# Performance work log

Measured on AMD Instinct MI355X. Metric: run time of the kernel, lower is better.

## Reference

```python
import jax, jax.numpy as jnp
import numpy as np

NUM_CLUSTERS = 8
KMEANS_ITERS = 10  # fixed Lloyd iterations (deterministic stand-in for sklearn KMeans)


def _pairwise_sqdist(x, cent):
    # x: [N, C], cent: [K, C] -> [N, K]
    return (jnp.sum(x * x, axis=1, keepdims=True)
            - 2.0 * (x @ cent.T)
            + jnp.sum(cent * cent, axis=1)[None, :])


def _kmeans_labels(x):
    # x: [N, C] -> labels [N] int32. Deterministic init: first K points.
    K = NUM_CLUSTERS
    cent0 = x[:K]

    def step(cent, _):
        d = _pairwise_sqdist(x, cent)                      # [N, K]
        lab = jnp.argmin(d, axis=1)                        # [N]
        oh = jax.nn.one_hot(lab, K, dtype=x.dtype)         # [N, K]
        cnt = oh.sum(axis=0)                               # [K]
        sums = oh.T @ x                                    # [K, C]
        new = jnp.where(cnt[:, None] > 0,
                        sums / jnp.maximum(cnt, 1.0)[:, None],
                        cent)
        return new, None

    cent, _ = jax.lax.scan(step, cent0, None, length=KMEANS_ITERS)
    return jnp.argmin(_pairwise_sqdist(x, cent), axis=1)


def setup_inputs() -> dict:
    key = jax.random.key(0)
    feature_map = jax.random.normal(key, (32, 256, 64, 64), dtype=jnp.float32)
    return {"feature_map": feature_map}


def reference(feature_map):
    B, C, H, W = feature_map.shape
    K = NUM_CLUSTERS
    # (B, C, H, W) -> (B, N, C) with N = H*W
    feats = feature_map.reshape(B, C, H * W).transpose(0, 2, 1)
    # Cluster assignments are non-differentiable constants (torch uses .detach())
    labels = jax.vmap(_kmeans_labels)(jax.lax.stop_gradient(feats))   # [B, N]
    oh = jax.nn.one_hot(labels, K, dtype=feats.dtype)                 # [B, N, K]
    cnt = oh.sum(axis=1)                                              # [B, K]
    sums = jnp.einsum('bnk,bnc->bkc', oh, feats)                      # [B, K, C]
    # empty cluster -> zeros, matching torch fallback
    clustered = jnp.where(cnt[..., None] > 0,
                          sums / jnp.maximum(cnt, 1.0)[..., None],
                          0.0)
    return clustered  # [B, K, C]
```

## Files before the change

kernel.cpp:

```cpp
#include <hip/hip_runtime.h>
#include <stdint.h>

#define NB   32
#define NC   256
#define NPTS 4096
#define KCL  8
#define KC   384
#define NPANEL 11
#define BSTRIDE 388

__device__ float np_sumsq_avx512(const float* sh) {
  float half[2];
  #pragma unroll
  for (int h = 0; h < 2; ++h) {
    const float* ap = sh + h * 128;
    float rv[16];
    #pragma unroll
    for (int l = 0; l < 16; ++l) {
      float q[8];
      #pragma unroll
      for (int j = 0; j < 8; ++j) {
        float e = ap[16 * j + l];
        q[j] = __fmul_rn(e, e);
      }
      rv[l] = __fadd_rn(__fadd_rn(__fadd_rn(q[0], q[1]), __fadd_rn(q[2], q[3])),
                        __fadd_rn(__fadd_rn(q[4], q[5]), __fadd_rn(q[6], q[7])));
    }
    float t1[8];
    #pragma unroll
    for (int l = 0; l < 8; ++l) t1[l] = __fadd_rn(rv[l], rv[l + 8]);
    float t2[4];
    #pragma unroll
    for (int l = 0; l < 4; ++l) t2[l] = __fadd_rn(t1[l], t1[l + 2 + 2]);
    float t3[2];
    #pragma unroll
    for (int l = 0; l < 2; ++l) t3[l] = __fadd_rn(t2[l], t2[l + 2]);
    half[h] = __fadd_rn(t3[0], t3[1]);
  }
  return __fadd_rn(half[0], half[1]);
}

__global__ __launch_bounds__(256) void k_init(const float* __restrict__ X,
                                              float* __restrict__ centT,
                                              float* __restrict__ cnorm) {
  const int b = blockIdx.x >> 3, k = blockIdx.x & 7, c = threadIdx.x;
  __shared__ float sarr[NC];
  float v = X[(size_t)b * NC * NPTS + (size_t)c * NPTS + k];
  centT[(b * NC + c) * KCL + k] = v;
  sarr[c] = v;
  __syncthreads();
  if (c == 0) cnorm[b * KCL + k] = np_sumsq_avx512(sarr);
}

__global__ __launch_bounds__(256) void k_assign(const float* __restrict__ X,
                                                const float* __restrict__ centT,
                                                const float* __restrict__ cnorm,
                                                int* __restrict__ lab) {
  const int blk = blockIdx.x;
  const int b   = blk >> 4;
  const int n0  = (blk & 15) << 8;
  const int t   = threadIdx.x;

  const float* Xp = X + (size_t)b * NC * NPTS + n0 + t;
  const float4* cw = (const float4*)(centT + (size_t)b * NC * KCL);

  float cnf[KCL];
  #pragma unroll
  for (int k = 0; k < KCL; ++k) cnf[k] = cnorm[b * KCL + k];

  float a = 0.f;
  float bb[KCL];
  #pragma unroll
  for (int k = 0; k < KCL; ++k) bb[k] = 0.f;

  #pragma unroll 8
  for (int c = 0; c < NC; ++c) {
    float x = Xp[(size_t)c * NPTS];
    a = __fadd_rn(a, __fmul_rn(x, x));
    float4 c0 = cw[c * 2], c1 = cw[c * 2 + 1];
    bb[0] = __builtin_fmaf(x, c0.x, bb[0]);
    bb[1] = __builtin_fmaf(x, c0.y, bb[1]);
    bb[2] = __builtin_fmaf(x, c0.z, bb[2]);
    bb[3] = __builtin_fmaf(x, c0.w, bb[3]);
    bb[4] = __builtin_fmaf(x, c1.x, bb[4]);
    bb[5] = __builtin_fmaf(x, c1.y, bb[5]);
    bb[6] = __builtin_fmaf(x, c1.z, bb[6]);
    bb[7] = __builtin_fmaf(x, c1.w, bb[7]);
  }

  int lb = 0; float best = 3.4e38f;
  #pragma unroll
  for (int k = 0; k < KCL; ++k) {
    float d = __fadd_rn(__fsub_rn(a, __fmul_rn(2.0f, bb[k])), cnf[k]);
    if (d < best) { best = d; lb = k; }
  }
  lab[b * NPTS + n0 + t] = lb;
}

__global__ __launch_bounds__(256) void k_psum(const float* __restrict__ X,
                                              const int* __restrict__ lab,
                                              float* __restrict__ pp,
                                              int* __restrict__ pc) {
  const int blk = blockIdx.x;
  const int b = blk / 88, r = blk % 88, panel = r >> 3, cg = r & 7;
  const int p0 = panel * KC;
  const int len = (panel < 10) ? KC : (NPTS - 10 * KC);
  const int t = threadIdx.x, k = t & 7, cl = t >> 3, lane = t & 63;

  __shared__ __align__(16) float buf[32 * BSTRIDE];
  __shared__ int perm[KC];
  __shared__ int wcnt[6][KCL];
  __shared__ int cbase[6][KCL];
  __shared__ int offs[KCL], hist[KCL];

  const float* Xb = X + (size_t)b * NC * NPTS + (size_t)(cg * 32) * NPTS + p0;
  if (len == KC) {
    #pragma unroll
    for (int i2 = 0; i2 < 12; ++i2) {
      int i = i2 * 256 + t;
      int c = i / 96, q4 = i - c * 96;
      float4 v = *(const float4*)(Xb + (size_t)c * NPTS + q4 * 4);
      *(float4*)&buf[c * BSTRIDE + q4 * 4] = v;
    }
  } else {
    #pragma unroll
    for (int i2 = 0; i2 < 8; ++i2) {
      int i = i2 * 256 + t;
      int c = i >> 6, q4 = i & 63;
      float4 v = *(const float4*)(Xb + (size_t)c * NPTS + q4 * 4);
      *(float4*)&buf[c * BSTRIDE + q4 * 4] = v;
    }
  }

  const int* Lb = lab + b * NPTS + p0;
  const uint64_t lt = (1ull << lane) - 1ull;
  int ml0, ml1, rk0 = 0, rk1 = 0;
  {
    const int q = t;
    ml0 = (q < len) ? Lb[q] : -1;
    const int chunk = q >> 6;
    #pragma unroll
    for (int kk = 0; kk < KCL; ++kk) {
      uint64_t m = __ballot(ml0 == kk);
      if (lane == 0) wcnt[chunk][kk] = (int)__popcll(m);
      if (ml0 == kk) rk0 = (int)__popcll(m & lt);
    }
  }
  {
    const int q = 256 + t;
    ml1 = (q < len) ? Lb[q] : -1;
    const int chunk = q >> 6;
    #pragma unroll
    for (int kk = 0; kk < KCL; ++kk) {
      uint64_t m = __ballot(ml1 == kk);
      if (lane == 0 && chunk < 6) wcnt[chunk][kk] = (int)__popcll(m);
      if (ml1 == kk) rk1 = (int)__popcll(m & lt);
    }
  }
  __syncthreads();
  if (t == 0) {
    int rr = 0;
    for (int kk = 0; kk < KCL; ++kk) {
      int s = 0;
      #pragma unroll
      for (int ch = 0; ch < 6; ++ch) { cbase[ch][kk] = rr + s; s += wcnt[ch][kk]; }
      offs[kk] = rr; hist[kk] = s; rr += s;
    }
  }
  __syncthreads();
  if (ml0 >= 0) perm[cbase[t >> 6][ml0] + rk0] = t;
  if (ml1 >= 0) perm[cbase[(256 + t) >> 6][ml1] + rk1] = 256 + t;
  __syncthreads();

  const int base = offs[k], n = hist[k];
  const float* bp = &buf[cl * BSTRIDE];
  float pa = 0.f;
  #pragma unroll 4
  for (int i = 0; i < n; ++i) {
    int p = perm[base + i];
    pa = __fadd_rn(pa, bp[p]);
  }
  pp[(size_t)((b * NPANEL + panel) * KCL + k) * NC + cg * 32 + cl] = pa;
  if (cl == 0) pc[(b * NPANEL + panel) * KCL + k] = n;
}

__global__ __launch_bounds__(256) void k_combine(const float* __restrict__ pp,
                                                 const int* __restrict__ pc,
                                                 float* __restrict__ centT,
                                                 float* __restrict__ cnorm) {
  const int b = blockIdx.x >> 3, k = blockIdx.x & 7, c = threadIdx.x;
  float C = 0.f;
  int cnt = 0;
  for (int pnl = 0; pnl < NPANEL; ++pnl) {
    C = __fadd_rn(C, pp[(size_t)((b * NPANEL + pnl) * KCL + k) * NC + c]);
    cnt += pc[(b * NPANEL + pnl) * KCL + k];
  }
  const float mean = __fdiv_rn(C, (float)((cnt > 0) ? cnt : 1));
  const int ci = (b * NC + c) * KCL + k;
  float nv = (cnt > 0) ? mean : centT[ci];
  centT[ci] = nv;
  __shared__ float sarr[NC];
  sarr[c] = nv;
  __syncthreads();
  if (c == 0) cnorm[b * KCL + k] = np_sumsq_avx512(sarr);
}

__global__ __launch_bounds__(256) void k_out(const float* __restrict__ pp,
                                             const int* __restrict__ pc,
                                             float* __restrict__ out) {
  const int b = blockIdx.x >> 3, k = blockIdx.x & 7, c = threadIdx.x;
  float C = 0.f;
  int cnt = 0;
  for (int pnl = 0; pnl < NPANEL; ++pnl) {
    C = __fadd_rn(C, pp[(size_t)((b * NPANEL + pnl) * KCL + k) * NC + c]);
    cnt += pc[(b * NPANEL + pnl) * KCL + k];
  }
  out[(b * KCL + k) * NC + c] =
      (cnt > 0) ? __fdiv_rn(C, (float)cnt) : 0.0f;
}

extern "C" void kernel_launch(void* const* d_in, const int* in_sizes, int n_in,
                              void* d_out, int out_size, void* d_ws, size_t ws_size,
                              hipStream_t stream) {
  const float* X = (const float*)d_in[0];
  float* out = (float*)d_out;

  float* centT = (float*)d_ws;
  float* cnorm = centT + (size_t)NB * NC * KCL;
  int*   lab   = (int*)(cnorm + NB * KCL);
  float* pp    = (float*)(lab + (size_t)NB * NPTS);
  int*   pc    = (int*)(pp + (size_t)NB * NPANEL * KCL * NC);

  k_init<<<NB * KCL, 256, 0, stream>>>(X, centT, cnorm);
  for (int it = 0; it < 10; ++it) {
    k_assign<<<NB * 16, 256, 0, stream>>>(X, centT, cnorm, lab);
    k_psum<<<NB * NPANEL * KCL, 256, 0, stream>>>(X, lab, pp, pc);
    k_combine<<<NB * KCL, 256, 0, stream>>>(pp, pc, centT, cnorm);
  }
  k_assign<<<NB * 16, 256, 0, stream>>>(X, centT, cnorm, lab);
  k_psum<<<NB * NPANEL * KCL, 256, 0, stream>>>(X, lab, pp, pc);
  k_out<<<NB * KCL, 256, 0, stream>>>(pp, pc, out);
}
```

Baseline: 741.1 us.

## Fuse centroid update into assign kernel and halve psum shared buffer

Removes the separate k_combine kernel. Each assign block now recomputes the new centroids and their norms from the panel partial sums, stages the centroids in shared memory, and ping-pongs between two centroid buffers. k_psum now loads its panel in two halves into a half-sized shared buffer, which lowers LDS use and should allow more blocks per CU, at the cost of extra barriers. The work of combining centroids is repeated by the 16 blocks per batch, and the norm is computed by only 8 threads per block.

```diff
diff --git a/kernel.cpp b/kernel.cpp
--- a/kernel.cpp
+++ b/kernel.cpp
@@ -7,7 +7,8 @@
 #define KCL  8
 #define KC   384
 #define NPANEL 11
-#define BSTRIDE 388
+#define HALF0 192
+#define BSTR  196
 
 __device__ float np_sumsq_avx512(const float* sh) {
   float half[2];
@@ -40,44 +41,106 @@
   return __fadd_rn(half[0], half[1]);
 }
 
+__device__ float np_sumsq_avx512_s8(const float* base, int k) {
+  float half[2];
+  #pragma unroll
+  for (int h = 0; h < 2; ++h) {
+    float rv[16];
+    #pragma unroll
+    for (int l = 0; l < 16; ++l) {
+      float q[8];
+      #pragma unroll
+      for (int j = 0; j < 8; ++j) {
+        float e = base[(h * 128 + 16 * j + l) * KCL + k];
+        q[j] = __fmul_rn(e, e);
+      }
+      rv[l] = __fadd_rn(__fadd_rn(__fadd_rn(q[0], q[1]), __fadd_rn(q[2], q[3])),
+                        __fadd_rn(__fadd_rn(q[4], q[5]), __fadd_rn(q[6], q[7])));
+    }
+    float t1[8];
+    #pragma unroll
+    for (int l = 0; l < 8; ++l) t1[l] = __fadd_rn(rv[l], rv[l + 8]);
+    float t2[4];
+    #pragma unroll
+    for (int l = 0; l < 4; ++l) t2[l] = __fadd_rn(t1[l], t1[l + 2 + 2]);
+    float t3[2];
+    #pragma unroll
+    for (int l = 0; l < 2; ++l) t3[l] = __fadd_rn(t2[l], t2[l + 2]);
+    half[h] = __fadd_rn(t3[0], t3[1]);
+  }
+  return __fadd_rn(half[0], half[1]);
+}
+
 __global__ __launch_bounds__(256) void k_init(const float* __restrict__ X,
-                                              float* __restrict__ centT,
-                                              float* __restrict__ cnorm) {
+                                              float* __restrict__ cent0,
+                                              float* __restrict__ cnorm0) {
   const int b = blockIdx.x >> 3, k = blockIdx.x & 7, c = threadIdx.x;
   __shared__ float sarr[NC];
   float v = X[(size_t)b * NC * NPTS + (size_t)c * NPTS + k];
-  centT[(b * NC + c) * KCL + k] = v;
+  cent0[(b * NC + c) * KCL + k] = v;
   sarr[c] = v;
   __syncthreads();
-  if (c == 0) cnorm[b * KCL + k] = np_sumsq_avx512(sarr);
+  if (c == 0) cnorm0[b * KCL + k] = np_sumsq_avx512(sarr);
 }
 
 __global__ __launch_bounds__(256) void k_assign(const float* __restrict__ X,
-                                                const float* __restrict__ centT,
-                                                const float* __restrict__ cnorm,
-                                                int* __restrict__ lab) {
+                                                const float* __restrict__ pp,
+                                                const int* __restrict__ pc,
+                                                const float* __restrict__ centPrev,
+                                                float* __restrict__ centCur,
+                                                const float* __restrict__ cnorm0,
+                                                int* __restrict__ lab,
+                                                int it) {
   const int blk = blockIdx.x;
   const int b   = blk >> 4;
   const int n0  = (blk & 15) << 8;
   const int t   = threadIdx.x;
 
+  __shared__ __align__(16) float centL[NC * KCL];
+  __shared__ float cnfL[KCL];
+
+  if (it == 0) {
+    const float4* cp = (const float4*)(centPrev + (size_t)b * NC * KCL);
+    #pragma unroll
+    for (int i2 = 0; i2 < 2; ++i2)
+      ((float4*)centL)[i2 * 256 + t] = cp[i2 * 256 + t];
+    if (t < KCL) cnfL[t] = cnorm0[b * KCL + t];
+  } else {
+    const int c = t;
+    #pragma unroll
+    for (int k = 0; k < KCL; ++k) {
+      float C = 0.f; int cnt = 0;
+      for (int pnl = 0; pnl < NPANEL; ++pnl) {
+        C = __fadd_rn(C, pp[(size_t)((b * NPANEL + pnl) * KCL + k) * NC + c]);
+        cnt += pc[(b * NPANEL + pnl) * KCL + k];
+      }
+      const float mean = __fdiv_rn(C, (float)((cnt > 0) ? cnt : 1));
+      const int ci = (b * NC + c) * KCL + k;
+      float nv = (cnt > 0) ? mean : centPrev[ci];
+      centCur[ci] = nv;
+      centL[c * KCL + k] = nv;
+    }
+    __syncthreads();
+    if (t < KCL) cnfL[t] = np_sumsq_avx512_s8(centL, t);
+  }
+  __syncthreads();
+
+  float cnf[KCL];
+  #pragma unroll
+  for (int k = 0; k < KCL; ++k) cnf[k] = cnfL[k];
+
   const float* Xp = X + (size_t)b * NC * NPTS + n0 + t;
-  const float4* cw = (const float4*)(centT + (size_t)b * NC * KCL);
-
-  float cnf[KCL];
-  #pragma unroll
-  for (int k = 0; k < KCL; ++k) cnf[k] = cnorm[b * KCL + k];
-
   float a = 0.f;
   float bb[KCL];
   #pragma unroll
   for (int k = 0; k < KCL; ++k) bb[k] = 0.f;
+  const float4* cL4 = (const float4*)centL;
 
   #pragma unroll 8
   for (int c = 0; c < NC; ++c) {
     float x = Xp[(size_t)c * NPTS];
     a = __fadd_rn(a, __fmul_rn(x, x));
-    float4 c0 = cw[c * 2], c1 = cw[c * 2 + 1];
+    float4 c0 = cL4[c * 2], c1 = cL4[c * 2 + 1];
     bb[0] = __builtin_fmaf(x, c0.x, bb[0]);
     bb[1] = __builtin_fmaf(x, c0.y, bb[1]);
     bb[2] = __builtin_fmaf(x, c0.z, bb[2]);
@@ -107,29 +170,20 @@
   const int len = (panel < 10) ? KC : (NPTS - 10 * KC);
   const int t = threadIdx.x, k = t & 7, cl = t >> 3, lane = t & 63;
 
-  __shared__ __align__(16) float buf[32 * BSTRIDE];
+  __shared__ __align__(16) float buf[32 * BSTR];
   __shared__ int perm[KC];
   __shared__ int wcnt[6][KCL];
   __shared__ int cbase[6][KCL];
   __shared__ int offs[KCL], hist[KCL];
 
   const float* Xb = X + (size_t)b * NC * NPTS + (size_t)(cg * 32) * NPTS + p0;
-  if (len == KC) {
-    #pragma unroll
-    for (int i2 = 0; i2 < 12; ++i2) {
-      int i = i2 * 256 + t;
-      int c = i / 96, q4 = i - c * 96;
-      float4 v = *(const float4*)(Xb + (size_t)c * NPTS + q4 * 4);
-      *(float4*)&buf[c * BSTRIDE + q4 * 4] = v;
-    }
-  } else {
-    #pragma unroll
-    for (int i2 = 0; i2 < 8; ++i2) {
-      int i = i2 * 256 + t;
-      int c = i >> 6, q4 = i & 63;
-      float4 v = *(const float4*)(Xb + (size_t)c * NPTS + q4 * 4);
-      *(float4*)&buf[c * BSTRIDE + q4 * 4] = v;
-    }
+
+  #pragma unroll
+  for (int i2 = 0; i2 < 6; ++i2) {
+    int i = i2 * 256 + t;
+    int c = i / 48, q4 = i - c * 48;
+    *(float4*)&buf[c * BSTR + q4 * 4] =
+        *(const float4*)(Xb + (size_t)c * NPTS + q4 * 4);
   }
 
   const int* Lb = lab + b * NPTS + p0;
@@ -173,36 +227,34 @@
   __syncthreads();
 
   const int base = offs[k], n = hist[k];
-  const float* bp = &buf[cl * BSTRIDE];
+  const int nh0 = cbase[3][k] - offs[k];
+  const float* bp = &buf[cl * BSTR];
   float pa = 0.f;
   #pragma unroll 4
-  for (int i = 0; i < n; ++i) {
+  for (int i = 0; i < nh0; ++i) {
     int p = perm[base + i];
     pa = __fadd_rn(pa, bp[p]);
   }
+  __syncthreads();
+
+  const int nf4 = (len - HALF0) >> 2;
+  #pragma unroll
+  for (int i2 = 0; i2 < 6; ++i2) {
+    int i = i2 * 256 + t;
+    int c = i / 48, q4 = i - c * 48;
+    if (q4 < nf4)
+      *(float4*)&buf[c * BSTR + q4 * 4] =
+          *(const float4*)(Xb + (size_t)c * NPTS + HALF0 + q4 * 4);
+  }
+  __syncthreads();
+
+  #pragma unroll 4
+  for (int i = nh0; i < n; ++i) {
+    int p = perm[base + i] - HALF0;
+    pa = __fadd_rn(pa, bp[p]);
+  }
   pp[(size_t)((b * NPANEL + panel) * KCL + k) * NC + cg * 32 + cl] = pa;
   if (cl == 0) pc[(b * NPANEL + panel) * KCL + k] = n;
-}
-
-__global__ __launch_bounds__(256) void k_combine(const float* __restrict__ pp,
-                                                 const int* __restrict__ pc,
-                                                 float* __restrict__ centT,
-                                                 float* __restrict__ cnorm) {
-  const int b = blockIdx.x >> 3, k = blockIdx.x & 7, c = threadIdx.x;
-  float C = 0.f;
-  int cnt = 0;
-  for (int pnl = 0; pnl < NPANEL; ++pnl) {
-    C = __fadd_rn(C, pp[(size_t)((b * NPANEL + pnl) * KCL + k) * NC + c]);
-    cnt += pc[(b * NPANEL + pnl) * KCL + k];
-  }
-  const float mean = __fdiv_rn(C, (float)((cnt > 0) ? cnt : 1));
-  const int ci = (b * NC + c) * KCL + k;
-  float nv = (cnt > 0) ? mean : centT[ci];
-  centT[ci] = nv;
-  __shared__ float sarr[NC];
-  sarr[c] = nv;
-  __syncthreads();
-  if (c == 0) cnorm[b * KCL + k] = np_sumsq_avx512(sarr);
 }
 
 __global__ __launch_bounds__(256) void k_out(const float* __restrict__ pp,
@@ -225,19 +277,21 @@
   const float* X = (const float*)d_in[0];
   float* out = (float*)d_out;
 
-  float* centT = (float*)d_ws;
-  float* cnorm = centT + (size_t)NB * NC * KCL;
-  int*   lab   = (int*)(cnorm + NB * KCL);
-  float* pp    = (float*)(lab + (size_t)NB * NPTS);
-  int*   pc    = (int*)(pp + (size_t)NB * NPANEL * KCL * NC);
-
-  k_init<<<NB * KCL, 256, 0, stream>>>(X, centT, cnorm);
-  for (int it = 0; it < 10; ++it) {
-    k_assign<<<NB * 16, 256, 0, stream>>>(X, centT, cnorm, lab);
+  float* cent0  = (float*)d_ws;
+  float* cent1  = cent0 + (size_t)NB * NC * KCL;
+  float* cnorm0 = cent1 + (size_t)NB * NC * KCL;
+  int*   lab    = (int*)(cnorm0 + NB * KCL);
+  float* pp     = (float*)(lab + (size_t)NB * NPTS);
+  int*   pc     = (int*)(pp + (size_t)NB * NPANEL * KCL * NC);
+
+  float* cent[2] = {cent0, cent1};
+
+  k_init<<<NB * KCL, 256, 0, stream>>>(X, cent0, cnorm0);
+  for (int it = 0; it <= 10; ++it) {
+    float* prev = (it == 0) ? cent0 : cent[(it - 1) & 1];
+    float* cur  = cent[it & 1];
+    k_assign<<<NB * 16, 256, 0, stream>>>(X, pp, pc, prev, cur, cnorm0, lab, it);
     k_psum<<<NB * NPANEL * KCL, 256, 0, stream>>>(X, lab, pp, pc);
-    k_combine<<<NB * KCL, 256, 0, stream>>>(pp, pc, centT, cnorm);
-  }
-  k_assign<<<NB * 16, 256, 0, stream>>>(X, centT, cnorm, lab);
-  k_psum<<<NB * NPANEL * KCL, 256, 0, stream>>>(X, lab, pp, pc);
+  }
   k_out<<<NB * KCL, 256, 0, stream>>>(pp, pc, out);
 }
```

Result: no change. 743.9 us (+0.4%).
